# Kernel tuning notes

Hardware: AMD Instinct MI355X
Metric: run time of the kernel (lower is better)

## Reference

```python
import jax, jax.numpy as jnp
import numpy as np

E = 384      # n_embed
H = 6        # n_head
HS = E // H  # head_size = 64
B = 64
T = 256      # == block_size
FF = 4 * E


def _layernorm(x, g, b, eps=1e-5):
    m = x.mean(-1, keepdims=True)
    v = ((x - m) ** 2).mean(-1, keepdims=True)
    return (x - m) / jnp.sqrt(v + eps) * g + b


def _mha(q_in, k_in, v_in, wq, bq, wk, bk, wv, bv, pw, pb):
    # Faithful to source: scale uses q_in's last dim (n_embed=384), NOT head_size,
    # and the causal tril mask is applied even in cross-attention.
    scale = q_in.shape[-1] ** -0.5
    q = jnp.einsum('bte,hes->bhts', q_in, wq) + bq[None, :, None, :]  # [B,H,T1,HS]
    k = jnp.einsum('bue,hes->bhus', k_in, wk) + bk[None, :, None, :]  # [B,H,T2,HS]
    v = jnp.einsum('bue,hes->bhus', v_in, wv) + bv[None, :, None, :]
    wei = jnp.einsum('bhts,bhus->bhtu', q, k) * scale                 # [B,H,T1,T2]
    T1, T2 = q_in.shape[1], k_in.shape[1]
    mask = jnp.tril(jnp.ones((T1, T2), dtype=bool))
    wei = jnp.where(mask[None, None], wei, -jnp.inf)
    wei = jax.nn.softmax(wei, axis=-1)
    out = jnp.einsum('bhtu,bhus->bths', wei, v)                       # [B,T1,H,HS]
    out = out.reshape(out.shape[0], out.shape[1], -1)                 # concat heads
    return out @ pw + pb


def setup_inputs() -> dict:
    key = jax.random.key(0)
    ks = jax.random.split(key, 32)
    s = 0.02
    d = {
        'encode_output': jax.random.normal(ks[0], (B, T, E), jnp.float32),
        'x': jax.random.normal(ks[1], (B, T, E), jnp.float32),
    }
    i = 2
    for p in ('sa1', 'sa2'):
        d[p + '_wq'] = jax.random.normal(ks[i], (H, E, HS), jnp.float32) * s; i += 1
        d[p + '_bq'] = jnp.zeros((H, HS), jnp.float32)
        d[p + '_wk'] = jax.random.normal(ks[i], (H, E, HS), jnp.float32) * s; i += 1
        d[p + '_bk'] = jnp.zeros((H, HS), jnp.float32)
        d[p + '_wv'] = jax.random.normal(ks[i], (H, E, HS), jnp.float32) * s; i += 1
        d[p + '_bv'] = jnp.zeros((H, HS), jnp.float32)
        d[p + '_pw'] = jax.random.normal(ks[i], (E, E), jnp.float32) * s; i += 1
        d[p + '_pb'] = jnp.zeros((E,), jnp.float32)
    d['ff_w1'] = jax.random.normal(ks[i], (E, FF), jnp.float32) * s; i += 1
    d['ff_b1'] = jnp.zeros((FF,), jnp.float32)
    d['ff_w2'] = jax.random.normal(ks[i], (FF, E), jnp.float32) * s; i += 1
    d['ff_b2'] = jnp.zeros((E,), jnp.float32)
    for n in ('ln1', 'ln2', 'ln3'):
        d[n + '_g'] = jnp.ones((E,), jnp.float32)
        d[n + '_b'] = jnp.zeros((E,), jnp.float32)
    return d


def reference(encode_output, x,
              sa1_wq, sa1_bq, sa1_wk, sa1_bk, sa1_wv, sa1_bv, sa1_pw, sa1_pb,
              sa2_wq, sa2_bq, sa2_wk, sa2_bk, sa2_wv, sa2_bv, sa2_pw, sa2_pb,
              ff_w1, ff_b1, ff_w2, ff_b2,
              ln1_g, ln1_b, ln2_g, ln2_b, ln3_g, ln3_b):
    # masked self-attention + add&norm
    a1 = _mha(x, x, x, sa1_wq, sa1_bq, sa1_wk, sa1_bk, sa1_wv, sa1_bv, sa1_pw, sa1_pb)
    o1 = _layernorm(x + a1, ln1_g, ln1_b)
    # cross-attention (q=o1, k=v=encode_output) + add&norm
    a2 = _mha(o1, encode_output, encode_output,
              sa2_wq, sa2_bq, sa2_wk, sa2_bk, sa2_wv, sa2_bv, sa2_pw, sa2_pb)
    o2 = _layernorm(o1 + a2, ln2_g, ln2_b)
    # FFN + add&norm
    f = jax.nn.relu(o2 @ ff_w1 + ff_b1) @ ff_w2 + ff_b2
    return _layernorm(o2 + f, ln3_g, ln3_b)
```

## Files before the change

### kernel.cpp

```cpp
#include <hip/hip_runtime.h>

typedef __attribute__((ext_vector_type(8))) short bf16x8;
typedef __attribute__((ext_vector_type(4))) float f32x4;

__device__ __forceinline__ float b2f(ushort b) {
    union { unsigned int u; float f; } x;
    x.u = ((unsigned int)b) << 16;
    return x.f;
}
__device__ __forceinline__ ushort f2b(float f) {
    union { float f; unsigned int u; } x;
    x.f = f;
    unsigned int r = x.u + 0x7fffu + ((x.u >> 16) & 1u);
    return (ushort)(r >> 16);
}
__device__ __forceinline__ int4 pack8(float4 a, float4 b) {
    union { int4 v; ushort u[8]; } r;
    r.u[0] = f2b(a.x); r.u[1] = f2b(a.y); r.u[2] = f2b(a.z); r.u[3] = f2b(a.w);
    r.u[4] = f2b(b.x); r.u[5] = f2b(b.y); r.u[6] = f2b(b.z); r.u[7] = f2b(b.w);
    return r.v;
}
__device__ __forceinline__ void gl2lds16(const ushort* g, ushort* l) {
    __builtin_amdgcn_global_load_lds(
        (const __attribute__((address_space(1))) void*)g,
        (__attribute__((address_space(3))) void*)l, 16, 0, 0);
}

__global__ __launch_bounds__(256) void gemm_bt(
    const ushort* __restrict__ A, const ushort* __restrict__ Bt,
    ushort* __restrict__ C, const float* __restrict__ bias,
    const ushort* __restrict__ resb, const float* __restrict__ resf,
    int M, int N, int K, int relu)
{
    __shared__ __align__(16) ushort As[128 * 32];
    __shared__ __align__(16) ushort Bs[128 * 32];
    const int tid  = threadIdx.x;
    const int wave = tid >> 6, lane = tid & 63;
    const int wm = wave >> 1, wn = wave & 1;
    const int qd = lane >> 4, lc = lane & 15;
    const int row0 = blockIdx.y * 128, col0 = blockIdx.x * 128;
    const int sr = lane >> 2;
    const int sc = (lane & 3) * 8;

    const ushort* Ag  = A  + (size_t)(row0 + wave * 32 + sr) * K + sc;
    const ushort* Ag2 = Ag + (size_t)16 * K;
    const ushort* Bg  = Bt + (size_t)(col0 + wave * 32 + sr) * K + sc;
    const ushort* Bg2 = Bg + (size_t)16 * K;
    ushort* Asd = &As[wave * 1024];
    ushort* Bsd = &Bs[wave * 1024];

    f32x4 acc[4][4];
#pragma unroll
    for (int i = 0; i < 4; i++)
#pragma unroll
        for (int j = 0; j < 4; j++) acc[i][j] = 0.0f;

    for (int k0 = 0; k0 < K; k0 += 32) {
        gl2lds16(Ag  + k0, Asd);
        gl2lds16(Ag2 + k0, Asd + 512);
        gl2lds16(Bg  + k0, Bsd);
        gl2lds16(Bg2 + k0, Bsd + 512);
        __syncthreads();

        bf16x8 af[4], bfr[4];
#pragma unroll
        for (int mi = 0; mi < 4; mi++)
            af[mi] = *(const bf16x8*)&As[(wm * 64 + mi * 16 + lc) * 32 + qd * 8];
#pragma unroll
        for (int ni = 0; ni < 4; ni++)
            bfr[ni] = *(const bf16x8*)&Bs[(wn * 64 + ni * 16 + lc) * 32 + qd * 8];
#pragma unroll
        for (int mi = 0; mi < 4; mi++)
#pragma unroll
            for (int ni = 0; ni < 4; ni++)
                acc[mi][ni] = __builtin_amdgcn_mfma_f32_16x16x32_bf16(
                    af[mi], bfr[ni], acc[mi][ni], 0, 0, 0);
        __syncthreads();
    }

#pragma unroll
    for (int mi = 0; mi < 4; mi++) {
#pragma unroll
        for (int r = 0; r < 4; r++) {
            int grow = row0 + wm * 64 + mi * 16 + qd * 4 + r;
#pragma unroll
            for (int ni = 0; ni < 4; ni++) {
                int gcol = col0 + wn * 64 + ni * 16 + lc;
                float v = acc[mi][ni][r];
                if (bias) v += bias[gcol];
                if (resb) v += b2f(resb[(size_t)grow * N + gcol]);
                if (resf) v += resf[(size_t)grow * N + gcol];
                if (relu) v = fmaxf(v, 0.0f);
                C[(size_t)grow * N + gcol] = f2b(v);
            }
        }
    }
}

__global__ __launch_bounds__(256) void gemm_n64(
    const ushort* __restrict__ A, const ushort* __restrict__ Bt,
    ushort* __restrict__ C, const float* __restrict__ bias,
    const ushort* __restrict__ resb, const float* __restrict__ resf,
    int M, int N, int K, int relu)
{
    __shared__ __align__(16) ushort As[128 * 32];
    __shared__ __align__(16) ushort Bs[64 * 32];
    const int tid  = threadIdx.x;
    const int wave = tid >> 6, lane = tid & 63;
    const int qd = lane >> 4, lc = lane & 15;
    const int row0 = blockIdx.y * 128, col0 = blockIdx.x * 64;
    const int sr = lane >> 2;
    const int sc = (lane & 3) * 8;

    const ushort* Ag  = A  + (size_t)(row0 + wave * 32 + sr) * K + sc;
    const ushort* Ag2 = Ag + (size_t)16 * K;
    const ushort* Bg  = Bt + (size_t)(col0 + wave * 16 + sr) * K + sc;
    ushort* Asd = &As[wave * 1024];
    ushort* Bsd = &Bs[wave * 512];

    f32x4 acc[2][4];
#pragma unroll
    for (int i = 0; i < 2; i++)
#pragma unroll
        for (int j = 0; j < 4; j++) acc[i][j] = 0.0f;

    for (int k0 = 0; k0 < K; k0 += 32) {
        gl2lds16(Ag  + k0, Asd);
        gl2lds16(Ag2 + k0, Asd + 512);
        gl2lds16(Bg  + k0, Bsd);
        __syncthreads();

        bf16x8 af[2], bfr[4];
#pragma unroll
        for (int mi = 0; mi < 2; mi++)
            af[mi] = *(const bf16x8*)&As[(wave * 32 + mi * 16 + lc) * 32 + qd * 8];
#pragma unroll
        for (int ni = 0; ni < 4; ni++)
            bfr[ni] = *(const bf16x8*)&Bs[(ni * 16 + lc) * 32 + qd * 8];
#pragma unroll
        for (int mi = 0; mi < 2; mi++)
#pragma unroll
            for (int ni = 0; ni < 4; ni++)
                acc[mi][ni] = __builtin_amdgcn_mfma_f32_16x16x32_bf16(
                    af[mi], bfr[ni], acc[mi][ni], 0, 0, 0);
        __syncthreads();
    }

#pragma unroll
    for (int mi = 0; mi < 2; mi++) {
#pragma unroll
        for (int r = 0; r < 4; r++) {
            int grow = row0 + wave * 32 + mi * 16 + qd * 4 + r;
#pragma unroll
            for (int ni = 0; ni < 4; ni++) {
                int gcol = col0 + ni * 16 + lc;
                float v = acc[mi][ni][r];
                if (bias) v += bias[gcol];
                if (resb) v += b2f(resb[(size_t)grow * N + gcol]);
                if (resf) v += resf[(size_t)grow * N + gcol];
                if (relu) v = fmaxf(v, 0.0f);
                C[(size_t)grow * N + gcol] = f2b(v);
            }
        }
    }
}

__global__ __launch_bounds__(256) void attn(
    const ushort* __restrict__ q, int qstr,
    const ushort* __restrict__ k, int kstr,
    const ushort* __restrict__ v, int vstr,
    ushort* __restrict__ out)
{
    __shared__ __align__(16) ushort Qs[64 * 72];
    __shared__ __align__(16) ushort Kc[64 * 72];
    __shared__ __align__(16) ushort Vc[64 * 72];
    __shared__ __align__(16) ushort Ps[64 * 264];

    const int tid = threadIdx.x;
    const int wave = tid >> 6, lane = tid & 63;
    const int qd = lane >> 4, lc = lane & 15;
    const int b = blockIdx.z, h = blockIdx.y, t0 = blockIdx.x * 64;
    const int hc = h * 64;
    const float scale = 0.051031036307982884f;

    {
        int r = tid >> 2, c = (tid & 3) * 16;
        int4 q0 = *(const int4*)&q[(size_t)(b * 256 + t0 + r) * qstr + hc + c];
        int4 q1 = *(const int4*)&q[(size_t)(b * 256 + t0 + r) * qstr + hc + c + 8];
        *(int4*)&Qs[r * 72 + c] = q0;
        *(int4*)&Qs[r * 72 + c + 8] = q1;
    }

    f32x4 accS[16];
#pragma unroll
    for (int j = 0; j < 16; j++) accS[j] = 0.0f;

    for (int uc = 0; uc < 4; uc++) {
        int r = tid >> 2, c = (tid & 3) * 16;
        int4 k0v = *(const int4*)&k[(size_t)(b * 256 + uc * 64 + r) * kstr + hc + c];
        int4 k1v = *(const int4*)&k[(size_t)(b * 256 + uc * 64 + r) * kstr + hc + c + 8];
        __syncthreads();
        *(int4*)&Kc[r * 72 + c] = k0v;
        *(int4*)&Kc[r * 72 + c + 8] = k1v;
        __syncthreads();
#pragma unroll
        for (int s0 = 0; s0 < 64; s0 += 32) {
            bf16x8 a = *(const bf16x8*)&Qs[(wave * 16 + lc) * 72 + s0 + qd * 8];
#pragma unroll
            for (int ni = 0; ni < 4; ni++) {
                bf16x8 bb = *(const bf16x8*)&Kc[(ni * 16 + lc) * 72 + s0 + qd * 8];
                accS[uc * 4 + ni] =
                    __builtin_amdgcn_mfma_f32_16x16x32_bf16(a, bb, accS[uc * 4 + ni], 0, 0, 0);
            }
        }
    }

#pragma unroll
    for (int rr = 0; rr < 4; rr++) {
        int t = t0 + wave * 16 + qd * 4 + rr;
        float pv[16];
        float mx = -3.0e38f;
#pragma unroll
        for (int j = 0; j < 16; j++) {
            int u = (j >> 2) * 64 + (j & 3) * 16 + lc;
            float s = accS[j][rr] * scale;
            s = (u <= t) ? s : -3.0e38f;
            pv[j] = s;
            mx = fmaxf(mx, s);
        }
#pragma unroll
        for (int m = 1; m < 16; m <<= 1) mx = fmaxf(mx, __shfl_xor(mx, m, 16));
        float sum = 0.0f;
#pragma unroll
        for (int j = 0; j < 16; j++) { float p = __expf(pv[j] - mx); pv[j] = p; sum += p; }
#pragma unroll
        for (int m = 1; m < 16; m <<= 1) sum += __shfl_xor(sum, m, 16);
        float inv = 1.0f / sum;
#pragma unroll
        for (int j = 0; j < 16; j++) {
            int u = (j >> 2) * 64 + (j & 3) * 16 + lc;
            Ps[(wave * 16 + qd * 4 + rr) * 264 + u] = f2b(pv[j] * inv);
        }
    }

    f32x4 accO[4];
#pragma unroll
    for (int j = 0; j < 4; j++) accO[j] = 0.0f;
    for (int uc = 0; uc < 4; uc++) {
        int r = tid >> 2, s0 = (tid & 3) * 16;
        int4 v0 = *(const int4*)&v[(size_t)(b * 256 + uc * 64 + r) * vstr + hc + s0];
        int4 v1 = *(const int4*)&v[(size_t)(b * 256 + uc * 64 + r) * vstr + hc + s0 + 8];
        __syncthreads();
        {
            const ushort* t0p = (const ushort*)&v0;
            const ushort* t1p = (const ushort*)&v1;
#pragma unroll
            for (int j = 0; j < 8; j++) Vc[(s0 + j) * 72 + r] = t0p[j];
#pragma unroll
            for (int j = 0; j < 8; j++) Vc[(s0 + 8 + j) * 72 + r] = t1p[j];
        }
        __syncthreads();
#pragma unroll
        for (int u0 = 0; u0 < 64; u0 += 32) {
            bf16x8 a = *(const bf16x8*)&Ps[(wave * 16 + lc) * 264 + uc * 64 + u0 + qd * 8];
#pragma unroll
            for (int ni = 0; ni < 4; ni++) {
                bf16x8 bb = *(const bf16x8*)&Vc[(ni * 16 + lc) * 72 + u0 + qd * 8];
                accO[ni] = __builtin_amdgcn_mfma_f32_16x16x32_bf16(a, bb, accO[ni], 0, 0, 0);
            }
        }
    }

#pragma unroll
    for (int ni = 0; ni < 4; ni++)
#pragma unroll
        for (int rr = 0; rr < 4; rr++) {
            int t = t0 + wave * 16 + qd * 4 + rr;
            out[(size_t)(b * 256 + t) * 384 + hc + ni * 16 + lc] = f2b(accO[ni][rr]);
        }
}

__global__ __launch_bounds__(256) void lnorm(
    const ushort* __restrict__ in, const float* __restrict__ g,
    const float* __restrict__ be, ushort* __restrict__ outb,
    float* __restrict__ outf)
{
    const int wave = threadIdx.x >> 6, lane = threadIdx.x & 63;
    const int row = blockIdx.x * 4 + wave;
    const ushort* r = in + (size_t)row * 384;
    float x[6], s1 = 0.0f, s2 = 0.0f;
#pragma unroll
    for (int j = 0; j < 6; j++) {
        x[j] = b2f(r[j * 64 + lane]);
        s1 += x[j]; s2 += x[j] * x[j];
    }
#pragma unroll
    for (int m = 1; m < 64; m <<= 1) {
        s1 += __shfl_xor(s1, m, 64);
        s2 += __shfl_xor(s2, m, 64);
    }
    float mean = s1 * (1.0f / 384.0f);
    float var  = s2 * (1.0f / 384.0f) - mean * mean;
    float rstd = rsqrtf(var + 1e-5f);
#pragma unroll
    for (int j = 0; j < 6; j++) {
        float y = (x[j] - mean) * rstd * g[j * 64 + lane] + be[j * 64 + lane];
        if (outb) outb[(size_t)row * 384 + j * 64 + lane] = f2b(y);
        if (outf) outf[(size_t)row * 384 + j * 64 + lane] = y;
    }
}

__global__ __launch_bounds__(256) void f32cvt(const float* __restrict__ in,
                                             ushort* __restrict__ out)
{
    size_t i = ((size_t)blockIdx.x * 256 + threadIdx.x) * 8;
    float4 a = *(const float4*)(in + i);
    float4 b = *(const float4*)(in + i + 4);
    *(int4*)(out + i) = pack8(a, b);
}

__global__ __launch_bounds__(256) void transp_t(
    const float* __restrict__ in, ushort* __restrict__ out, int R, int C)
{
    __shared__ float t[32][33];
    const int tx = threadIdx.x & 31, ty = threadIdx.x >> 5;
    const int c0 = blockIdx.x * 32, r0 = blockIdx.y * 32;
#pragma unroll
    for (int i = 0; i < 32; i += 8)
        t[ty + i][tx] = in[(size_t)(r0 + ty + i) * C + c0 + tx];
    __syncthreads();
#pragma unroll
    for (int i = 0; i < 32; i += 8)
        out[(size_t)(c0 + ty + i) * R + r0 + tx] = f2b(t[tx][ty + i]);
}

__global__ __launch_bounds__(256) void pack_qkv_t(
    const float* __restrict__ wq, const float* __restrict__ wk,
    const float* __restrict__ wv, ushort* __restrict__ Wt)
{
    __shared__ float t[32][33];
    const int tx = threadIdx.x & 31, ty = threadIdx.x >> 5;
    const int e0 = blockIdx.x * 32, s0 = blockIdx.y * 32;
    const int z = blockIdx.z, seg = z / 6, h = z - seg * 6;
    const float* w = (seg == 0) ? wq : (seg == 1) ? wk : wv;
    const float* wh = w + (size_t)h * 384 * 64;
#pragma unroll
    for (int i = 0; i < 32; i += 8)
        t[ty + i][tx] = wh[(size_t)(e0 + ty + i) * 64 + s0 + tx];
    __syncthreads();
    const int nbase = seg * 384 + h * 64 + s0;
#pragma unroll
    for (int i = 0; i < 32; i += 8)
        Wt[(size_t)(nbase + ty + i) * 384 + e0 + tx] = f2b(t[tx][ty + i]);
}

__global__ __launch_bounds__(256) void biaspack(
    const float* __restrict__ q1, const float* __restrict__ k1, const float* __restrict__ v1,
    const float* __restrict__ q2, const float* __restrict__ k2, const float* __restrict__ v2,
    float* __restrict__ b1, float* __restrict__ b2)
{
    int i = blockIdx.x * 256 + threadIdx.x;
    if (i >= 2304) return;
    int grp = i / 1152, r = i - grp * 1152;
    int seg = r / 384, nn = r - seg * 384;
    const float* src = grp == 0 ? (seg == 0 ? q1 : seg == 1 ? k1 : v1)
                                : (seg == 0 ? q2 : seg == 1 ? k2 : v2);
    (grp == 0 ? b1 : b2)[r] = src[nn];
}

extern "C" void kernel_launch(void* const* d_in, const int* in_sizes, int n_in,
                              void* d_out, int out_size, void* d_ws, size_t ws_size,
                              hipStream_t stream)
{
    const float* enc = (const float*)d_in[0];
    const float* x   = (const float*)d_in[1];
    const float* s1wq = (const float*)d_in[2];  const float* s1bq = (const float*)d_in[3];
    const float* s1wk = (const float*)d_in[4];  const float* s1bk = (const float*)d_in[5];
    const float* s1wv = (const float*)d_in[6];  const float* s1bv = (const float*)d_in[7];
    const float* s1pw = (const float*)d_in[8];  const float* s1pb = (const float*)d_in[9];
    const float* s2wq = (const float*)d_in[10]; const float* s2bq = (const float*)d_in[11];
    const float* s2wk = (const float*)d_in[12]; const float* s2bk = (const float*)d_in[13];
    const float* s2wv = (const float*)d_in[14]; const float* s2bv = (const float*)d_in[15];
    const float* s2pw = (const float*)d_in[16]; const float* s2pb = (const float*)d_in[17];
    const float* fw1 = (const float*)d_in[18];  const float* fb1 = (const float*)d_in[19];
    const float* fw2 = (const float*)d_in[20];  const float* fb2 = (const float*)d_in[21];
    const float* g1 = (const float*)d_in[22];   const float* be1 = (const float*)d_in[23];
    const float* g2 = (const float*)d_in[24];   const float* be2 = (const float*)d_in[25];
    const float* g3 = (const float*)d_in[26];   const float* be3 = (const float*)d_in[27];

    if (ws_size < 80216064u) return;

    ushort* wsp = (ushort*)d_ws;
    ushort* qkv1 = wsp;
    ushort* q2   = wsp;
    ushort* kv2  = wsp + 6291456;
    ushort* h1   = wsp;
    ushort* att  = wsp + 18874368;
    ushort* xb   = wsp + 18874368;
    ushort* tmp  = wsp + 25165824;
    ushort* o1b  = wsp + 31457280;
    ushort* W1   = wsp + 37748736;
    ushort* W2   = W1 + 442368;
    ushort* pw1t = W2 + 442368;
    ushort* pw2t = pw1t + 147456;
    ushort* w1t  = pw2t + 147456;
    ushort* w2t  = w1t + 589824;

    ushort* encb = (ushort*)d_out;
    ushort* o2b  = (ushort*)d_out;
    float* bias1 = (float*)((ushort*)d_out + 6291456);
    float* bias2 = bias1 + 1152;

    f32cvt<<<dim3(3072), dim3(256), 0, stream>>>(x, xb);
    f32cvt<<<dim3(3072), dim3(256), 0, stream>>>(enc, encb);
    pack_qkv_t<<<dim3(12, 2, 18), dim3(256), 0, stream>>>(s1wq, s1wk, s1wv, W1);
    pack_qkv_t<<<dim3(12, 2, 18), dim3(256), 0, stream>>>(s2wq, s2wk, s2wv, W2);
    biaspack<<<dim3(9), dim3(256), 0, stream>>>(s1bq, s1bk, s1bv, s2bq, s2bk, s2bv, bias1, bias2);
    transp_t<<<dim3(12, 12), dim3(256), 0, stream>>>(s1pw, pw1t, 384, 384);
    transp_t<<<dim3(12, 12), dim3(256), 0, stream>>>(s2pw, pw2t, 384, 384);
    transp_t<<<dim3(48, 12), dim3(256), 0, stream>>>(fw1, w1t, 384, 1536);
    transp_t<<<dim3(12, 48), dim3(256), 0, stream>>>(fw2, w2t, 1536, 384);

    gemm_bt<<<dim3(9, 128), dim3(256), 0, stream>>>(xb, W1, qkv1, bias1, nullptr, nullptr, 16384, 1152, 384, 0);
    attn<<<dim3(4, 6, 64), dim3(256), 0, stream>>>(qkv1, 1152, qkv1 + 384, 1152, qkv1 + 768, 1152, att);
    gemm_n64<<<dim3(6, 128), dim3(256), 0, stream>>>(att, pw1t, tmp, s1pb, nullptr, x, 16384, 384, 384, 0);
    lnorm<<<dim3(4096), dim3(256), 0, stream>>>(tmp, g1, be1, o1b, nullptr);

    gemm_n64<<<dim3(6, 128), dim3(256), 0, stream>>>(o1b, W2, q2, bias2, nullptr, nullptr, 16384, 384, 384, 0);
    gemm_n64<<<dim3(12, 128), dim3(256), 0, stream>>>(encb, W2 + 147456, kv2, bias2 + 384, nullptr, nullptr, 16384, 768, 384, 0);
    attn<<<dim3(4, 6, 64), dim3(256), 0, stream>>>(q2, 384, kv2, 768, kv2 + 384, 768, att);
    gemm_n64<<<dim3(6, 128), dim3(256), 0, stream>>>(att, pw2t, tmp, s2pb, o1b, nullptr, 16384, 384, 384, 0);
    lnorm<<<dim3(4096), dim3(256), 0, stream>>>(tmp, g2, be2, o2b, nullptr);

    gemm_bt<<<dim3(12, 128), dim3(256), 0, stream>>>(o2b, w1t, h1, fb1, nullptr, nullptr, 16384, 1536, 384, 1);
    gemm_n64<<<dim3(6, 128), dim3(256), 0, stream>>>(h1, w2t, tmp, fb2, o2b, nullptr, 16384, 384, 1536, 0);
    lnorm<<<dim3(4096), dim3(256), 0, stream>>>(tmp, g3, be3, nullptr, (float*)d_out);
}
```

Before: 535.4 us.

## Double GEMM K-step to 64 per barrier and merge Q2/KV2 projections

Both GEMM kernels now load two 32-wide K slices into separate LDS buffers per iteration. This halves the number of barrier pairs and issues more loads in flight before each sync. A new gemm_dual kernel computes the cross-attention Q projection and the encoder K/V projection in a single launch, choosing operands per block. This saves one launch and lets the two small grids fill the GPU together, at the cost of doubled LDS per block, which may lower occupancy. The code assumes K is a multiple of 64.

```diff
diff --git a/kernel.cpp b/kernel.cpp
--- a/kernel.cpp
+++ b/kernel.cpp
@@ -32,8 +32,8 @@
     const ushort* __restrict__ resb, const float* __restrict__ resf,
     int M, int N, int K, int relu)
 {
-    __shared__ __align__(16) ushort As[128 * 32];
-    __shared__ __align__(16) ushort Bs[128 * 32];
+    __shared__ __align__(16) ushort As[2][128 * 32];
+    __shared__ __align__(16) ushort Bs[2][128 * 32];
     const int tid  = threadIdx.x;
     const int wave = tid >> 6, lane = tid & 63;
     const int wm = wave >> 1, wn = wave & 1;
@@ -46,8 +46,6 @@
     const ushort* Ag2 = Ag + (size_t)16 * K;
     const ushort* Bg  = Bt + (size_t)(col0 + wave * 32 + sr) * K + sc;
     const ushort* Bg2 = Bg + (size_t)16 * K;
-    ushort* Asd = &As[wave * 1024];
-    ushort* Bsd = &Bs[wave * 1024];
 
     f32x4 acc[4][4];
 #pragma unroll
@@ -55,26 +53,33 @@
 #pragma unroll
         for (int j = 0; j < 4; j++) acc[i][j] = 0.0f;
 
-    for (int k0 = 0; k0 < K; k0 += 32) {
-        gl2lds16(Ag  + k0, Asd);
-        gl2lds16(Ag2 + k0, Asd + 512);
-        gl2lds16(Bg  + k0, Bsd);
-        gl2lds16(Bg2 + k0, Bsd + 512);
-        __syncthreads();
-
-        bf16x8 af[4], bfr[4];
-#pragma unroll
-        for (int mi = 0; mi < 4; mi++)
-            af[mi] = *(const bf16x8*)&As[(wm * 64 + mi * 16 + lc) * 32 + qd * 8];
-#pragma unroll
-        for (int ni = 0; ni < 4; ni++)
-            bfr[ni] = *(const bf16x8*)&Bs[(wn * 64 + ni * 16 + lc) * 32 + qd * 8];
-#pragma unroll
-        for (int mi = 0; mi < 4; mi++)
+    for (int k0 = 0; k0 < K; k0 += 64) {
+        gl2lds16(Ag  + k0,      &As[0][wave * 1024]);
+        gl2lds16(Ag2 + k0,      &As[0][wave * 1024 + 512]);
+        gl2lds16(Bg  + k0,      &Bs[0][wave * 1024]);
+        gl2lds16(Bg2 + k0,      &Bs[0][wave * 1024 + 512]);
+        gl2lds16(Ag  + k0 + 32, &As[1][wave * 1024]);
+        gl2lds16(Ag2 + k0 + 32, &As[1][wave * 1024 + 512]);
+        gl2lds16(Bg  + k0 + 32, &Bs[1][wave * 1024]);
+        gl2lds16(Bg2 + k0 + 32, &Bs[1][wave * 1024 + 512]);
+        __syncthreads();
+
+#pragma unroll
+        for (int c = 0; c < 2; c++) {
+            bf16x8 af[4], bfr[4];
+#pragma unroll
+            for (int mi = 0; mi < 4; mi++)
+                af[mi] = *(const bf16x8*)&As[c][(wm * 64 + mi * 16 + lc) * 32 + qd * 8];
 #pragma unroll
             for (int ni = 0; ni < 4; ni++)
-                acc[mi][ni] = __builtin_amdgcn_mfma_f32_16x16x32_bf16(
-                    af[mi], bfr[ni], acc[mi][ni], 0, 0, 0);
+                bfr[ni] = *(const bf16x8*)&Bs[c][(wn * 64 + ni * 16 + lc) * 32 + qd * 8];
+#pragma unroll
+            for (int mi = 0; mi < 4; mi++)
+#pragma unroll
+                for (int ni = 0; ni < 4; ni++)
+                    acc[mi][ni] = __builtin_amdgcn_mfma_f32_16x16x32_bf16(
+                        af[mi], bfr[ni], acc[mi][ni], 0, 0, 0);
+        }
         __syncthreads();
     }
 
@@ -103,8 +108,8 @@
     const ushort* __restrict__ resb, const float* __restrict__ resf,
     int M, int N, int K, int relu)
 {
-    __shared__ __align__(16) ushort As[128 * 32];
-    __shared__ __align__(16) ushort Bs[64 * 32];
+    __shared__ __align__(16) ushort As[2][128 * 32];
+    __shared__ __align__(16) ushort Bs[2][64 * 32];
     const int tid  = threadIdx.x;
     const int wave = tid >> 6, lane = tid & 63;
     const int qd = lane >> 4, lc = lane & 15;
@@ -115,8 +120,6 @@
     const ushort* Ag  = A  + (size_t)(row0 + wave * 32 + sr) * K + sc;
     const ushort* Ag2 = Ag + (size_t)16 * K;
     const ushort* Bg  = Bt + (size_t)(col0 + wave * 16 + sr) * K + sc;
-    ushort* Asd = &As[wave * 1024];
-    ushort* Bsd = &Bs[wave * 512];
 
     f32x4 acc[2][4];
 #pragma unroll
@@ -124,25 +127,31 @@
 #pragma unroll
         for (int j = 0; j < 4; j++) acc[i][j] = 0.0f;
 
-    for (int k0 = 0; k0 < K; k0 += 32) {
-        gl2lds16(Ag  + k0, Asd);
-        gl2lds16(Ag2 + k0, Asd + 512);
-        gl2lds16(Bg  + k0, Bsd);
-        __syncthreads();
-
-        bf16x8 af[2], bfr[4];
-#pragma unroll
-        for (int mi = 0; mi < 2; mi++)
-            af[mi] = *(const bf16x8*)&As[(wave * 32 + mi * 16 + lc) * 32 + qd * 8];
-#pragma unroll
-        for (int ni = 0; ni < 4; ni++)
-            bfr[ni] = *(const bf16x8*)&Bs[(ni * 16 + lc) * 32 + qd * 8];
-#pragma unroll
-        for (int mi = 0; mi < 2; mi++)
+    for (int k0 = 0; k0 < K; k0 += 64) {
+        gl2lds16(Ag  + k0,      &As[0][wave * 1024]);
+        gl2lds16(Ag2 + k0,      &As[0][wave * 1024 + 512]);
+        gl2lds16(Bg  + k0,      &Bs[0][wave * 512]);
+        gl2lds16(Ag  + k0 + 32, &As[1][wave * 1024]);
+        gl2lds16(Ag2 + k0 + 32, &As[1][wave * 1024 + 512]);
+        gl2lds16(Bg  + k0 + 32, &Bs[1][wave * 512]);
+        __syncthreads();
+
+#pragma unroll
+        for (int c = 0; c < 2; c++) {
+            bf16x8 af[2], bfr[4];
+#pragma unroll
+            for (int mi = 0; mi < 2; mi++)
+                af[mi] = *(const bf16x8*)&As[c][(wave * 32 + mi * 16 + lc) * 32 + qd * 8];
 #pragma unroll
             for (int ni = 0; ni < 4; ni++)
-                acc[mi][ni] = __builtin_amdgcn_mfma_f32_16x16x32_bf16(
-                    af[mi], bfr[ni], acc[mi][ni], 0, 0, 0);
+                bfr[ni] = *(const bf16x8*)&Bs[c][(ni * 16 + lc) * 32 + qd * 8];
+#pragma unroll
+            for (int mi = 0; mi < 2; mi++)
+#pragma unroll
+                for (int ni = 0; ni < 4; ni++)
+                    acc[mi][ni] = __builtin_amdgcn_mfma_f32_16x16x32_bf16(
+                        af[mi], bfr[ni], acc[mi][ni], 0, 0, 0);
+        }
         __syncthreads();
     }
 
@@ -159,6 +168,82 @@
                 if (resb) v += b2f(resb[(size_t)grow * N + gcol]);
                 if (resf) v += resf[(size_t)grow * N + gcol];
                 if (relu) v = fmaxf(v, 0.0f);
+                C[(size_t)grow * N + gcol] = f2b(v);
+            }
+        }
+    }
+}
+
+__global__ __launch_bounds__(256) void gemm_dual(
+    const ushort* __restrict__ A1, const ushort* __restrict__ B1t,
+    ushort* __restrict__ C1, const float* __restrict__ bias1, int N1,
+    const ushort* __restrict__ A2, const ushort* __restrict__ B2t,
+    ushort* __restrict__ C2, const float* __restrict__ bias2, int N2,
+    int split, int K)
+{
+    __shared__ __align__(16) ushort As[2][128 * 32];
+    __shared__ __align__(16) ushort Bs[2][64 * 32];
+    const int tid  = threadIdx.x;
+    const int wave = tid >> 6, lane = tid & 63;
+    const int qd = lane >> 4, lc = lane & 15;
+    const bool first = (int)blockIdx.x < split;
+    const ushort* A  = first ? A1 : A2;
+    const ushort* Bt = first ? B1t : B2t;
+    ushort* C        = first ? C1 : C2;
+    const float* bias = first ? bias1 : bias2;
+    const int N      = first ? N1 : N2;
+    const int col0   = (first ? blockIdx.x : blockIdx.x - split) * 64;
+    const int row0   = blockIdx.y * 128;
+    const int sr = lane >> 2;
+    const int sc = (lane & 3) * 8;
+
+    const ushort* Ag  = A  + (size_t)(row0 + wave * 32 + sr) * K + sc;
+    const ushort* Ag2 = Ag + (size_t)16 * K;
+    const ushort* Bg  = Bt + (size_t)(col0 + wave * 16 + sr) * K + sc;
+
+    f32x4 acc[2][4];
+#pragma unroll
+    for (int i = 0; i < 2; i++)
+#pragma unroll
+        for (int j = 0; j < 4; j++) acc[i][j] = 0.0f;
+
+    for (int k0 = 0; k0 < K; k0 += 64) {
+        gl2lds16(Ag  + k0,      &As[0][wave * 1024]);
+        gl2lds16(Ag2 + k0,      &As[0][wave * 1024 + 512]);
+        gl2lds16(Bg  + k0,      &Bs[0][wave * 512]);
+        gl2lds16(Ag  + k0 + 32, &As[1][wave * 1024]);
+        gl2lds16(Ag2 + k0 + 32, &As[1][wave * 1024 + 512]);
+        gl2lds16(Bg  + k0 + 32, &Bs[1][wave * 512]);
+        __syncthreads();
+
+#pragma unroll
+        for (int c = 0; c < 2; c++) {
+            bf16x8 af[2], bfr[4];
+#pragma unroll
+            for (int mi = 0; mi < 2; mi++)
+                af[mi] = *(const bf16x8*)&As[c][(wave * 32 + mi * 16 + lc) * 32 + qd * 8];
+#pragma unroll
+            for (int ni = 0; ni < 4; ni++)
+                bfr[ni] = *(const bf16x8*)&Bs[c][(ni * 16 + lc) * 32 + qd * 8];
+#pragma unroll
+            for (int mi = 0; mi < 2; mi++)
+#pragma unroll
+                for (int ni = 0; ni < 4; ni++)
+                    acc[mi][ni] = __builtin_amdgcn_mfma_f32_16x16x32_bf16(
+                        af[mi], bfr[ni], acc[mi][ni], 0, 0, 0);
+        }
+        __syncthreads();
+    }
+
+#pragma unroll
+    for (int mi = 0; mi < 2; mi++) {
+#pragma unroll
+        for (int r = 0; r < 4; r++) {
+            int grow = row0 + wave * 32 + mi * 16 + qd * 4 + r;
+#pragma unroll
+            for (int ni = 0; ni < 4; ni++) {
+                int gcol = col0 + ni * 16 + lc;
+                float v = acc[mi][ni][r] + bias[gcol];
                 C[(size_t)grow * N + gcol] = f2b(v);
             }
         }
@@ -426,8 +511,9 @@
     gemm_n64<<<dim3(6, 128), dim3(256), 0, stream>>>(att, pw1t, tmp, s1pb, nullptr, x, 16384, 384, 384, 0);
     lnorm<<<dim3(4096), dim3(256), 0, stream>>>(tmp, g1, be1, o1b, nullptr);
 
-    gemm_n64<<<dim3(6, 128), dim3(256), 0, stream>>>(o1b, W2, q2, bias2, nullptr, nullptr, 16384, 384, 384, 0);
-    gemm_n64<<<dim3(12, 128), dim3(256), 0, stream>>>(encb, W2 + 147456, kv2, bias2 + 384, nullptr, nullptr, 16384, 768, 384, 0);
+    gemm_dual<<<dim3(18, 128), dim3(256), 0, stream>>>(
+        o1b, W2, q2, bias2, 384,
+        encb, W2 + 147456, kv2, bias2 + 384, 768, 6, 384);
     attn<<<dim3(4, 6, 64), dim3(256), 0, stream>>>(q2, 384, kv2, 768, kv2 + 384, 768, att);
     gemm_n64<<<dim3(6, 128), dim3(256), 0, stream>>>(att, pw2t, tmp, s2pb, o1b, nullptr, 16384, 384, 384, 0);
     lnorm<<<dim3(4096), dim3(256), 0, stream>>>(tmp, g2, be2, o2b, nullptr);
```

Result: no change. 537.6 us (+0.4%).
